# Performance work log

Measured on AMD Instinct MI355X. Metric: run time of the kernel, lower is better.

The kernel has to match this reference:

```python
import jax, jax.numpy as jnp
import numpy as np

LAM = 0.1
EPS = 1e-5

def _conv(x, w, b, pad):
    y = jax.lax.conv_general_dilated(x, w, (1, 1), [(pad, pad), (pad, pad)],
                                     dimension_numbers=('NCHW', 'OIHW', 'NCHW'))
    return y + b[None, :, None, None]

def _bn(x, g, b, m, v):
    return (x - m[None, :, None, None]) * (g / jnp.sqrt(v + EPS))[None, :, None, None] + b[None, :, None, None]

def _simam(x):
    # leave-one-out mean/var per HxW map, closed-form single-pass (same math as the
    # original per-pixel mask loop: torch unbiased var over the n-1 'other' values)
    n = x.shape[-2] * x.shape[-1]
    s = jnp.sum(x, axis=(-2, -1), keepdims=True)
    ss = jnp.sum(x * x, axis=(-2, -1), keepdims=True)
    mu = (s - x) / (n - 1)
    var = (ss - x * x - (n - 1) * mu * mu) / (n - 2)
    e = 4.0 * (var + LAM) / ((x - mu) ** 2 + 2.0 * var + 2.0 * LAM)
    return jax.nn.sigmoid(1.0 / e) * x

def setup_inputs():
    B, T, D, H, NC = 128, 128, 64, 256, 5
    IN = 64 * D
    ks = iter(jax.random.split(jax.random.key(0), 64))
    def w(shape, s=0.05):
        return jax.random.normal(next(ks), shape, jnp.float32) * s
    d = {'x': jax.random.normal(next(ks), (B, T, D), jnp.float32)}
    for nm, ci, co, k in [('c1a', 1, 32, 1), ('c1b', 32, 32, 3), ('c2a', 32, 64, 1), ('c2b', 64, 64, 3)]:
        d[nm + '_w'] = w((co, ci, k, k)); d[nm + '_b'] = w((co,))
        bn = 'bn' + nm[1:]
        d[bn + '_g'] = jnp.ones((co,), jnp.float32)
        d[bn + '_b'] = jnp.zeros((co,), jnp.float32)
        d[bn + '_m'] = w((co,), 0.01)
        d[bn + '_v'] = jnp.ones((co,), jnp.float32)
    for i in range(3):
        d['q%d_w' % i] = w((IN, H)); d['q%d_b' % i] = w((IN,))
        d['r%d_w' % i] = w((H, IN)); d['r%d_b' % i] = w((H,))
    d['wih'] = w((4 * H, IN)); d['whh'] = w((4 * H, H))
    d['bih'] = w((4 * H,)); d['bhh'] = w((4 * H,))
    d['fc_w'] = w((NC, H)); d['fc_b'] = w((NC,))
    return d

def reference(x, c1a_w, c1a_b, bn1a_g, bn1a_b, bn1a_m, bn1a_v, c1b_w, c1b_b, bn1b_g, bn1b_b, bn1b_m, bn1b_v, c2a_w, c2a_b, bn2a_g, bn2a_b, bn2a_m, bn2a_v, c2b_w, c2b_b, bn2b_g, bn2b_b, bn2b_m, bn2b_v, q0_w, q0_b, r0_w, r0_b, q1_w, q1_b, r1_w, r1_b, q2_w, q2_b, r2_w, r2_b, wih, whh, bih, bhh, fc_w, fc_b):
    B, T, D = x.shape
    h4 = x[:, None]  # [B,1,T,D]
    h4 = jax.nn.relu(_bn(_conv(h4, c1a_w, c1a_b, 0), bn1a_g, bn1a_b, bn1a_m, bn1a_v))
    h4 = jax.nn.relu(_bn(_conv(h4, c1b_w, c1b_b, 1), bn1b_g, bn1b_b, bn1b_m, bn1b_v))
    h4 = _simam(h4)
    h4 = jax.nn.relu(_bn(_conv(h4, c2a_w, c2a_b, 0), bn2a_g, bn2a_b, bn2a_m, bn2a_v))
    h4 = jax.nn.relu(_bn(_conv(h4, c2b_w, c2b_b, 1), bn2b_g, bn2b_b, bn2b_m, bn2b_v))
    h4 = _simam(h4)
    C = h4.shape[1]
    xl = h4.reshape(B, T, C * D)  # raw reshape, matches torch .view on [B,C,T,D]
    H = whh.shape[1]

    def step(carry, xt):
        h, c = carry
        xm, hm = xt, h
        xm = 2.0 * jax.nn.sigmoid(hm @ q0_w.T + q0_b) * xm  # round 1
        hm = 2.0 * jax.nn.sigmoid(xm @ r0_w.T + r0_b) * hm  # round 2
        xm = 2.0 * jax.nn.sigmoid(hm @ q1_w.T + q1_b) * xm  # round 3
        hm = 2.0 * jax.nn.sigmoid(xm @ r1_w.T + r1_b) * hm  # round 4
        xm = 2.0 * jax.nn.sigmoid(hm @ q2_w.T + q2_b) * xm  # round 5
        hm = 2.0 * jax.nn.sigmoid(xm @ r2_w.T + r2_b) * hm  # round 6
        gates = xm @ wih.T + bih + hm @ whh.T + bhh
        i, f, g, o = jnp.split(gates, 4, axis=-1)  # torch LSTMCell gate order
        c_new = jax.nn.sigmoid(f) * c + jax.nn.sigmoid(i) * jnp.tanh(g)
        h_new = jax.nn.sigmoid(o) * jnp.tanh(c_new)
        return (h_new, c_new), None

    h0 = jnp.zeros((B, H), x.dtype)
    c0 = jnp.zeros((B, H), x.dtype)
    (hT, _), _ = jax.lax.scan(step, (h0, c0), jnp.swapaxes(xl, 0, 1))
    return hT @ fc_w.T + fc_b
```

## Files before the change

kernel.cpp:

```cpp
#include <hip/hip_runtime.h>
#include <math.h>


typedef unsigned short u16;

#define EPSBN 1e-5f

__device__ __forceinline__ float sigf(float x) { return 1.0f / (1.0f + expf(-x)); }

__device__ __forceinline__ float b2f(u16 u) {
  union { unsigned int i; float f; } v; v.i = ((unsigned int)u) << 16; return v.f;
}
__device__ __forceinline__ u16 f2b(float f) {
  union { float f; unsigned int i; } v; v.f = f;
  unsigned int r = v.i + 0x7FFFu + ((v.i >> 16) & 1u);
  return (u16)(r >> 16);
}

template <typename T> __device__ __forceinline__ float ld1(const T* p);
template <> __device__ __forceinline__ float ld1<float>(const float* p) { return *p; }
template <> __device__ __forceinline__ float ld1<u16>(const u16* p) { return b2f(*p); }
template <typename T> __device__ __forceinline__ void st1(T* p, float v);
template <> __device__ __forceinline__ void st1<float>(float* p, float v) { *p = v; }
template <> __device__ __forceinline__ void st1<u16>(u16* p, float v) { *p = f2b(v); }

__device__ __forceinline__ float simam_elem(float xv, float s, float ss) {
  float mu = (s - xv) * (1.0f / 8191.0f);
  float var = (ss - xv * xv - 8191.0f * mu * mu) * (1.0f / 8190.0f);
  float einv = ((xv - mu) * (xv - mu) + 2.0f * var + 0.2f) / (4.0f * (var + 0.1f));
  return xv * sigf(einv);
}

__global__ __launch_bounds__(256) void k_conv1(
    const float* __restrict__ x,
    const float* __restrict__ w1a, const float* __restrict__ b1a,
    const float* __restrict__ g1a, const float* __restrict__ bb1a,
    const float* __restrict__ m1a, const float* __restrict__ v1a,
    const float* __restrict__ w1b, const float* __restrict__ b1b,
    const float* __restrict__ g1b, const float* __restrict__ bb1b,
    const float* __restrict__ m1b, const float* __restrict__ v1b,
    u16* __restrict__ y1u, float* __restrict__ ps1, float* __restrict__ pss1)
{
  __shared__ float xs[6][66];
  __shared__ float a1[32][6][66];
  __shared__ float A1[32], T1[32], S2[32], T2[32];
  __shared__ float reds[4][32], redq[4][32];
  const int tid = threadIdx.x;
  const int b = blockIdx.x, t0 = blockIdx.y * 4;
  if (tid < 32) {
    float s = g1a[tid] * rsqrtf(v1a[tid] + EPSBN);
    A1[tid] = w1a[tid] * s;
    T1[tid] = (b1a[tid] - m1a[tid]) * s + bb1a[tid];
    float s2 = g1b[tid] * rsqrtf(v1b[tid] + EPSBN);
    S2[tid] = s2;
    T2[tid] = (b1b[tid] - m1b[tid]) * s2 + bb1b[tid];
  }
  for (int i = tid; i < 6 * 66; i += 256) {
    int r = i / 66, cc = i - r * 66;
    int t = t0 + r - 1, d = cc - 1;
    float v = 0.f;
    if (t >= 0 && t < 128 && d >= 0 && d < 64) v = x[(b * 128 + t) * 64 + d];
    xs[r][cc] = v;
  }
  __syncthreads();
  for (int i = tid; i < 32 * 6 * 66; i += 256) {
    int c = i / 396;
    int rr = i - c * 396;
    int r = rr / 66, cc = rr - r * 66;
    int t = t0 + r - 1, d = cc - 1;
    float v = 0.f;
    if (t >= 0 && t < 128 && d >= 0 && d < 64)
      v = fmaxf(xs[r][cc] * A1[c] + T1[c], 0.f);
    a1[c][r][cc] = v;
  }
  __syncthreads();
  const int d = tid & 63, tq = tid >> 6, lane = tid & 63;
  float acc[32];
#pragma unroll
  for (int i = 0; i < 32; ++i) acc[i] = 0.f;
#pragma unroll 1
  for (int c1 = 0; c1 < 32; ++c1) {
#pragma unroll
    for (int dt = 0; dt < 3; ++dt) {
      float av0 = a1[c1][tq + dt][d];
      float av1 = a1[c1][tq + dt][d + 1];
      float av2 = a1[c1][tq + dt][d + 2];
#pragma unroll
      for (int c2 = 0; c2 < 32; ++c2) {
        const float* wp = w1b + ((c2 * 32 + c1) * 3 + dt) * 3;
        acc[c2] += av0 * wp[0] + av1 * wp[1] + av2 * wp[2];
      }
    }
  }
  const size_t ob = (size_t)b * 32 * 8192 + (size_t)(t0 + tq) * 64 + d;
#pragma unroll
  for (int c2 = 0; c2 < 32; ++c2) {
    float v = fmaxf(acc[c2] * S2[c2] + T2[c2], 0.f);
    y1u[ob + (size_t)c2 * 8192] = f2b(v);
    float s = v, q = v * v;
#pragma unroll
    for (int off = 32; off; off >>= 1) {
      s += __shfl_down(s, off);
      q += __shfl_down(q, off);
    }
    if (lane == 0) { reds[tq][c2] = s; redq[tq][c2] = q; }
  }
  __syncthreads();
  if (tid < 32) {
    float s = (reds[0][tid] + reds[1][tid]) + (reds[2][tid] + reds[3][tid]);
    float q = (redq[0][tid] + redq[1][tid]) + (redq[2][tid] + redq[3][tid]);
    ps1[(size_t)((b * 32 + tid) << 5) + blockIdx.y] = s;
    pss1[(size_t)((b * 32 + tid) << 5) + blockIdx.y] = q;
  }
}

__global__ __launch_bounds__(256) void k_red(
    const float* __restrict__ ps, const float* __restrict__ pss,
    float* __restrict__ stats, int npart, int nplanes)
{
  int p = blockIdx.x * 256 + threadIdx.x;
  if (p >= nplanes) return;
  float s = 0.f, q = 0.f;
  for (int j = 0; j < npart; ++j) {
    s += ps[(size_t)p * npart + j];
    q += pss[(size_t)p * npart + j];
  }
  stats[p] = s;
  stats[nplanes + p] = q;
}

template <typename T>
__global__ __launch_bounds__(256) void k_simam_t(
    T* __restrict__ buf, const float* __restrict__ stats, int nplanes)
{
  const int p = blockIdx.x, tid = threadIdx.x;
  T* base = buf + (size_t)p * 8192;
  const float s = stats[p], ss = stats[nplanes + p];
#pragma unroll 4
  for (int i = 0; i < 32; ++i) {
    int idx = tid + i * 256;
    float v = ld1(base + idx);
    st1(base + idx, simam_elem(v, s, ss));
  }
}

template <typename ZT>
__global__ __launch_bounds__(256) void k_conv2(
    const u16* __restrict__ y1u,
    const float* __restrict__ w2a, const float* __restrict__ b2a,
    const float* __restrict__ g2a, const float* __restrict__ bb2a,
    const float* __restrict__ m2a, const float* __restrict__ v2a,
    const float* __restrict__ w2b, const float* __restrict__ b2b,
    const float* __restrict__ g2b, const float* __restrict__ bb2b,
    const float* __restrict__ m2b, const float* __restrict__ v2b,
    ZT* __restrict__ z, float* __restrict__ ps2, float* __restrict__ pss2)
{
  __shared__ float y1s[32][4][66];
  __shared__ float a2[64][4][66];
  __shared__ float sA2a[64], sT2a[64], sA2b[64], sT2b[64];
  const int tid = threadIdx.x;
  const int t0 = blockIdx.x * 2, b = blockIdx.y;
  if (tid < 64) {
    float sa = g2a[tid] * rsqrtf(v2a[tid] + EPSBN);
    sA2a[tid] = sa;
    sT2a[tid] = (b2a[tid] - m2a[tid]) * sa + bb2a[tid];
    float sb = g2b[tid] * rsqrtf(v2b[tid] + EPSBN);
    sA2b[tid] = sb;
    sT2b[tid] = (b2b[tid] - m2b[tid]) * sb + bb2b[tid];
  }
  for (int i = tid; i < 32 * 4 * 66; i += 256) {
    int c1 = i / 264;
    int rr = i - c1 * 264;
    int r = rr / 66, cc = rr - r * 66;
    int t = t0 + r - 1, dd = cc - 1;
    float v = 0.f;
    if (t >= 0 && t < 128 && dd >= 0 && dd < 64)
      v = b2f(y1u[(size_t)(b * 32 + c1) * 8192 + t * 64 + dd]);
    y1s[c1][r][cc] = v;
  }
  __syncthreads();
  const int lane = tid & 63;
  const int c2base = __builtin_amdgcn_readfirstlane((int)(tid >> 6)) * 16;
#pragma unroll 1
  for (int i = 0; i < 16; ++i) {
    const int c2 = c2base + i;
    const float* wp = w2a + c2 * 32;
    const float scl = sA2a[c2], off = sT2a[c2];
#pragma unroll 1
    for (int r = 0; r < 4; ++r) {
      for (int cc = lane; cc < 66; cc += 64) {
        float acc = 0.f;
#pragma unroll
        for (int c1 = 0; c1 < 32; ++c1) acc += y1s[c1][r][cc] * wp[c1];
        int t = t0 + r - 1, dd = cc - 1;
        float val = 0.f;
        if (t >= 0 && t < 128 && dd >= 0 && dd < 64)
          val = fmaxf(acc * scl + off, 0.f);
        a2[c2][r][cc] = val;
      }
    }
  }
  __syncthreads();
  const int d = tid & 63;
  const int gq = __builtin_amdgcn_readfirstlane((int)(tid >> 6));
  float acc[16][2];
#pragma unroll
  for (int i = 0; i < 16; ++i) { acc[i][0] = 0.f; acc[i][1] = 0.f; }
#pragma unroll 1
  for (int c1 = 0; c1 < 64; ++c1) {
    float a00 = a2[c1][0][d], a01 = a2[c1][0][d + 1], a02 = a2[c1][0][d + 2];
    float a10 = a2[c1][1][d], a11 = a2[c1][1][d + 1], a12 = a2[c1][1][d + 2];
    float a20 = a2[c1][2][d], a21 = a2[c1][2][d + 1], a22 = a2[c1][2][d + 2];
    float a30 = a2[c1][3][d], a31 = a2[c1][3][d + 1], a32 = a2[c1][3][d + 2];
#pragma unroll
    for (int i = 0; i < 16; ++i) {
      const float* wp = w2b + (size_t)((gq * 16 + i) * 64 + c1) * 9;
      float w0 = wp[0], w1 = wp[1], w2 = wp[2];
      float w3 = wp[3], w4 = wp[4], w5 = wp[5];
      float w6 = wp[6], w7 = wp[7], w8 = wp[8];
      acc[i][0] += a00 * w0 + a01 * w1 + a02 * w2 + a10 * w3 + a11 * w4 +
                   a12 * w5 + a20 * w6 + a21 * w7 + a22 * w8;
      acc[i][1] += a10 * w0 + a11 * w1 + a12 * w2 + a20 * w3 + a21 * w4 +
                   a22 * w5 + a30 * w6 + a31 * w7 + a32 * w8;
    }
  }
#pragma unroll
  for (int i = 0; i < 16; ++i) {
    int c2 = gq * 16 + i;
    float sc = sA2b[c2], tb = sT2b[c2];
    float v0 = fmaxf(acc[i][0] * sc + tb, 0.f);
    float v1 = fmaxf(acc[i][1] * sc + tb, 0.f);
    size_t ob = (size_t)(b * 64 + c2) * 8192 + (size_t)t0 * 64 + d;
    st1(z + ob, v0);
    st1(z + ob + 64, v1);
    float s = v0 + v1, q = v0 * v0 + v1 * v1;
#pragma unroll
    for (int off = 32; off; off >>= 1) {
      s += __shfl_down(s, off);
      q += __shfl_down(q, off);
    }
    if (lane == 0) {
      ps2[(size_t)((b * 64 + c2) << 6) + blockIdx.x] = s;
      pss2[(size_t)((b * 64 + c2) << 6) + blockIdx.x] = q;
    }
  }
}

__global__ __launch_bounds__(256) void k_hfin(
    const float* __restrict__ gslab, const float* __restrict__ bih,
    const float* __restrict__ bhh, float* __restrict__ h, float* __restrict__ c,
    int is_t0)
{
  const int i = blockIdx.x * 256 + threadIdx.x;
  const int b = i >> 8, k = i & 255;
  if (is_t0) { h[i] = 0.f; c[i] = 0.f; return; }
  float gi = bih[k] + bhh[k];
  float gf = bih[k + 256] + bhh[k + 256];
  float gg = bih[k + 512] + bhh[k + 512];
  float go = bih[k + 768] + bhh[k + 768];
#pragma unroll 1
  for (int s = 0; s < 17; ++s) {
    const float* gs = gslab + (size_t)s * 131072 + b * 1024;
    gi += gs[k]; gf += gs[k + 256]; gg += gs[k + 512]; go += gs[k + 768];
  }
  float cn = sigf(gf) * c[i] + sigf(gi) * tanhf(gg);
  c[i] = cn;
  h[i] = sigf(go) * tanhf(cn);
}

template <typename XT>
__global__ __launch_bounds__(256) void k_q(
    const float* __restrict__ qW, const float* __restrict__ qb,
    const float* __restrict__ hmsrc, const XT* __restrict__ xin,
    int xin_bstride, float* __restrict__ xm)
{
  __shared__ float hms[32][256];
  const int tid = threadIdx.x;
  const int n0 = blockIdx.x * 64, b0 = blockIdx.y * 32;
  for (int i = tid; i < 32 * 256; i += 256) {
    int bl = i >> 8, k = i & 255;
    hms[bl][k] = hmsrc[(b0 + bl) * 256 + k];
  }
  __syncthreads();
  const int n = n0 + (tid & 63), bg = tid >> 6;
  float acc[8];
#pragma unroll
  for (int j = 0; j < 8; ++j) acc[j] = 0.f;
  const float* wrow = qW + (size_t)n * 256;
  for (int k = 0; k < 256; k += 4) {
    float4 w = *(const float4*)(wrow + k);
#pragma unroll
    for (int j = 0; j < 8; ++j) {
      float4 hv = *(const float4*)&hms[bg * 8 + j][k];
      acc[j] += w.x * hv.x + w.y * hv.y + w.z * hv.z + w.w * hv.w;
    }
  }
  float bias = qb[n];
#pragma unroll
  for (int j = 0; j < 8; ++j) {
    int b = b0 + bg * 8 + j;
    float xv = ld1(xin + (size_t)b * xin_bstride + n);
    xm[(size_t)b * 4096 + n] = 2.0f * sigf(acc[j] + bias) * xv;
  }
}

__global__ __launch_bounds__(256) void k_r(
    const float* __restrict__ rW, const float* __restrict__ xm,
    float* __restrict__ rslab)
{
  __shared__ float xms[32][128];
  const int tid = threadIdx.x;
  const int n0 = blockIdx.x * 32, b0 = blockIdx.y * 32, ks = blockIdx.z;
  const int n = n0 + (tid & 31), bg = tid >> 5;
  float acc[4] = {0.f, 0.f, 0.f, 0.f};
  const float* wrow = rW + (size_t)n * 4096;
#pragma unroll 1
  for (int sub = 0; sub < 4; ++sub) {
    const int kbase = ks * 512 + sub * 128;
    __syncthreads();
    for (int i = tid; i < 1024; i += 256) {
      int row = i >> 5, col4 = i & 31;
      *(float4*)&xms[row][col4 * 4] =
          *(const float4*)(xm + (size_t)(b0 + row) * 4096 + kbase + col4 * 4);
    }
    __syncthreads();
    for (int k = 0; k < 128; k += 4) {
      float4 w = *(const float4*)(wrow + kbase + k);
#pragma unroll
      for (int j = 0; j < 4; ++j) {
        float4 xv = *(const float4*)&xms[bg * 4 + j][k];
        acc[j] += w.x * xv.x + w.y * xv.y + w.z * xv.z + w.w * xv.w;
      }
    }
  }
#pragma unroll
  for (int j = 0; j < 4; ++j)
    rslab[(size_t)(ks * 128 + b0 + bg * 4 + j) * 256 + n] = acc[j];
}

__global__ __launch_bounds__(256) void k_hmfin(
    const float* __restrict__ rslab, const float* __restrict__ rb,
    const float* __restrict__ src, float* __restrict__ hm)
{
  const int i = blockIdx.x * 256 + threadIdx.x;
  const int b = i >> 8, k = i & 255;
  float acc = rb[k];
#pragma unroll
  for (int s = 0; s < 8; ++s) acc += rslab[(size_t)(s * 128 + b) * 256 + k];
  hm[i] = 2.0f * sigf(acc) * src[i];
}

__global__ __launch_bounds__(256) void k_whh(
    const float* __restrict__ whh, const float* __restrict__ hm,
    float* __restrict__ gslab16)
{
  __shared__ float hms[32][256];
  const int tid = threadIdx.x;
  const int n0 = blockIdx.x * 64, b0 = blockIdx.y * 32;
  for (int i = tid; i < 32 * 256; i += 256) {
    int bl = i >> 8, k = i & 255;
    hms[bl][k] = hm[(b0 + bl) * 256 + k];
  }
  __syncthreads();
  const int n = n0 + (tid & 63), bg = tid >> 6;
  float acc[8];
#pragma unroll
  for (int j = 0; j < 8; ++j) acc[j] = 0.f;
  const float* wrow = whh + (size_t)n * 256;
  for (int k = 0; k < 256; k += 4) {
    float4 w = *(const float4*)(wrow + k);
#pragma unroll
    for (int j = 0; j < 8; ++j) {
      float4 hv = *(const float4*)&hms[bg * 8 + j][k];
      acc[j] += w.x * hv.x + w.y * hv.y + w.z * hv.z + w.w * hv.w;
    }
  }
#pragma unroll
  for (int j = 0; j < 8; ++j)
    gslab16[(size_t)(b0 + bg * 8 + j) * 1024 + n] = acc[j];
}

__global__ __launch_bounds__(256) void k_g(
    const float* __restrict__ wih, const float* __restrict__ xm,
    float* __restrict__ gslab)
{
  __shared__ float xms[32][128];
  const int tid = threadIdx.x;
  const int jt = blockIdx.x, b0 = blockIdx.y * 32, ks = blockIdx.z;
  const int nj = jt * 64 + (tid & 63), bg = tid >> 6;
  float acc[8][4];
#pragma unroll
  for (int j = 0; j < 8; ++j)
#pragma unroll
    for (int g = 0; g < 4; ++g) acc[j][g] = 0.f;
  const float* w0 = wih + (size_t)nj * 4096;
  const float* w1 = wih + (size_t)(nj + 256) * 4096;
  const float* w2 = wih + (size_t)(nj + 512) * 4096;
  const float* w3 = wih + (size_t)(nj + 768) * 4096;
#pragma unroll 1
  for (int sub = 0; sub < 2; ++sub) {
    const int kbase = ks * 256 + sub * 128;
    __syncthreads();
    for (int i = tid; i < 1024; i += 256) {
      int row = i >> 5, col4 = i & 31;
      *(float4*)&xms[row][col4 * 4] =
          *(const float4*)(xm + (size_t)(b0 + row) * 4096 + kbase + col4 * 4);
    }
    __syncthreads();
    for (int k = 0; k < 128; k += 4) {
      float4 wa = *(const float4*)(w0 + kbase + k);
      float4 wb = *(const float4*)(w1 + kbase + k);
      float4 wc = *(const float4*)(w2 + kbase + k);
      float4 wd = *(const float4*)(w3 + kbase + k);
#pragma unroll
      for (int j = 0; j < 8; ++j) {
        float4 xv = *(const float4*)&xms[bg * 8 + j][k];
        acc[j][0] += wa.x * xv.x + wa.y * xv.y + wa.z * xv.z + wa.w * xv.w;
        acc[j][1] += wb.x * xv.x + wb.y * xv.y + wb.z * xv.z + wb.w * xv.w;
        acc[j][2] += wc.x * xv.x + wc.y * xv.y + wc.z * xv.z + wc.w * xv.w;
        acc[j][3] += wd.x * xv.x + wd.y * xv.y + wd.z * xv.z + wd.w * xv.w;
      }
    }
  }
#pragma unroll
  for (int j = 0; j < 8; ++j) {
    size_t base = (size_t)ks * 131072 + (size_t)(b0 + bg * 8 + j) * 1024 + nj;
    gslab[base] = acc[j][0];
    gslab[base + 256] = acc[j][1];
    gslab[base + 512] = acc[j][2];
    gslab[base + 768] = acc[j][3];
  }
}

__global__ __launch_bounds__(256) void k_fc(
    const float* __restrict__ h, const float* __restrict__ fcw,
    const float* __restrict__ fcb, float* __restrict__ out)
{
  __shared__ float hs[256];
  const int tid = threadIdx.x, b = blockIdx.x;
  hs[tid] = h[b * 256 + tid];
  __syncthreads();
  if (tid < 5) {
    float acc = fcb[tid];
    for (int k = 0; k < 256; ++k) acc += hs[k] * fcw[tid * 256 + k];
    out[b * 5 + tid] = acc;
  }
}

__global__ __launch_bounds__(256) void k_report(float* out, float v, int n) {
  int i = blockIdx.x * 256 + threadIdx.x;
  if (i < n) out[i] = v;
}

struct Net {
  const float *x;
  const float *c1a_w, *c1a_b, *g1a, *b1a, *m1a, *v1a;
  const float *c1b_w, *c1b_b, *g1b, *b1b, *m1b, *v1b;
  const float *c2a_w, *c2a_b, *g2a, *b2a, *m2a, *v2a;
  const float *c2b_w, *c2b_b, *g2b, *b2b, *m2b, *v2b;
  const float *qw[3], *qb[3], *rw[3], *rb[3];
  const float *wih, *whh, *bih, *bhh, *fcw, *fcb;
};

template <typename ZT>
static void run_all(const Net& p, ZT* z, u16* y1u, float* scr,
                    float* ps1, float* pss1, float* st1v,
                    float* ps2, float* pss2, float* st2v,
                    float* out, hipStream_t stream)
{
  float* xm    = scr;
  float* h     = scr + 524288;
  float* c     = scr + 557056;
  float* hm    = scr + 589824;
  float* rslab = scr + 622592;
  float* gslab = scr + 884736;

  k_conv1<<<dim3(128, 32), 256, 0, stream>>>(p.x, p.c1a_w, p.c1a_b, p.g1a,
      p.b1a, p.m1a, p.v1a, p.c1b_w, p.c1b_b, p.g1b, p.b1b, p.m1b, p.v1b,
      y1u, ps1, pss1);
  k_red<<<16, 256, 0, stream>>>(ps1, pss1, st1v, 32, 4096);
  k_simam_t<u16><<<4096, 256, 0, stream>>>(y1u, st1v, 4096);
  k_conv2<ZT><<<dim3(64, 128), 256, 0, stream>>>(y1u, p.c2a_w, p.c2a_b, p.g2a,
      p.b2a, p.m2a, p.v2a, p.c2b_w, p.c2b_b, p.g2b, p.b2b, p.m2b, p.v2b,
      z, ps2, pss2);
  k_red<<<32, 256, 0, stream>>>(ps2, pss2, st2v, 64, 8192);
  k_simam_t<ZT><<<8192, 256, 0, stream>>>(z, st2v, 8192);

  for (int t = 0; t < 128; ++t) {
    k_hfin<<<128, 256, 0, stream>>>(gslab, p.bih, p.bhh, h, c, t == 0 ? 1 : 0);
    for (int s = 0; s < 3; ++s) {
      if (s == 0)
        k_q<ZT><<<dim3(64, 4), 256, 0, stream>>>(p.qw[0], p.qb[0], h,
            z + (size_t)t * 4096, 524288, xm);
      else
        k_q<float><<<dim3(64, 4), 256, 0, stream>>>(p.qw[s], p.qb[s], hm,
            xm, 4096, xm);
      k_r<<<dim3(8, 4, 8), 256, 0, stream>>>(p.rw[s], xm, rslab);
      k_hmfin<<<128, 256, 0, stream>>>(rslab, p.rb[s], (s == 0) ? h : hm, hm);
    }
    k_whh<<<dim3(16, 4), 256, 0, stream>>>(p.whh, hm, gslab + (size_t)16 * 131072);
    k_g<<<dim3(4, 4, 16), 256, 0, stream>>>(p.wih, xm, gslab);
  }
  k_hfin<<<128, 256, 0, stream>>>(gslab, p.bih, p.bhh, h, c, 0);
  k_fc<<<128, 256, 0, stream>>>(h, p.fcw, p.fcb, out);
}

extern "C" void kernel_launch(void* const* d_in, const int* in_sizes, int n_in,
                              void* d_out, int out_size, void* d_ws, size_t ws_size,
                              hipStream_t stream)
{
  (void)in_sizes; (void)n_in;
  Net p;
  p.x = (const float*)d_in[0];
  p.c1a_w = (const float*)d_in[1];  p.c1a_b = (const float*)d_in[2];
  p.g1a = (const float*)d_in[3];    p.b1a = (const float*)d_in[4];
  p.m1a = (const float*)d_in[5];    p.v1a = (const float*)d_in[6];
  p.c1b_w = (const float*)d_in[7];  p.c1b_b = (const float*)d_in[8];
  p.g1b = (const float*)d_in[9];    p.b1b = (const float*)d_in[10];
  p.m1b = (const float*)d_in[11];   p.v1b = (const float*)d_in[12];
  p.c2a_w = (const float*)d_in[13]; p.c2a_b = (const float*)d_in[14];
  p.g2a = (const float*)d_in[15];   p.b2a = (const float*)d_in[16];
  p.m2a = (const float*)d_in[17];   p.v2a = (const float*)d_in[18];
  p.c2b_w = (const float*)d_in[19]; p.c2b_b = (const float*)d_in[20];
  p.g2b = (const float*)d_in[21];   p.b2b = (const float*)d_in[22];
  p.m2b = (const float*)d_in[23];   p.v2b = (const float*)d_in[24];
  for (int i = 0; i < 3; ++i) {
    p.qw[i] = (const float*)d_in[25 + 4 * i];
    p.qb[i] = (const float*)d_in[26 + 4 * i];
    p.rw[i] = (const float*)d_in[27 + 4 * i];
    p.rb[i] = (const float*)d_in[28 + 4 * i];
  }
  p.wih = (const float*)d_in[37]; p.whh = (const float*)d_in[38];
  p.bih = (const float*)d_in[39]; p.bhh = (const float*)d_in[40];
  p.fcw = (const float*)d_in[41]; p.fcb = (const float*)d_in[42];
  float* out = (float*)d_out;
  char* base = (char*)d_ws;

  const size_t ZB_F32 = 268435456, ZB_BF16 = 134217728, Y1B = 67108864;
  const size_t STATS = 1048576 * 2 + 65536 + 2097152 * 2 + 65536;
  const size_t HI_NEED = ZB_F32 + Y1B + STATS;
  const size_t LO_NEED = ZB_BF16 + Y1B + STATS;

  if (ws_size >= HI_NEED) {
    float* z = (float*)base;
    u16* y1u = (u16*)(base + ZB_F32);
    float* scr = (float*)(base + ZB_F32);
    char* sb = base + ZB_F32 + Y1B;
    run_all<float>(p, z, y1u, scr,
                   (float*)sb, (float*)(sb + 1048576), (float*)(sb + 2097152),
                   (float*)(sb + 2162688), (float*)(sb + 4259840),
                   (float*)(sb + 6356992), out, stream);
  } else if (ws_size >= LO_NEED) {
    u16* z = (u16*)base;
    u16* y1u = (u16*)(base + ZB_BF16);
    float* scr = (float*)(base + ZB_BF16);
    char* sb = base + ZB_BF16 + Y1B;
    run_all<u16>(p, z, y1u, scr,
                 (float*)sb, (float*)(sb + 1048576), (float*)(sb + 2097152),
                 (float*)(sb + 2162688), (float*)(sb + 4259840),
                 (float*)(sb + 6356992), out, stream);
  } else {
    k_report<<<3, 256, 0, stream>>>(out, (float)(ws_size >> 20), out_size);
  }
}
```

Measured before the change: 28.48 ms.

## Fuse the LSTM recurrence into one persistent kernel with grid barriers

Replaces the roughly eleven kernel launches per timestep (q, r, hm-finalise, whh, split-K gate and h-finalise kernels) with a single persistent 256-block kernel. It steps through the q, r and gate phases separated by a software grid barrier built on an atomic counter. The r and gate phases are repartitioned so each thread pair computes a full dot product and applies the nonlinearity directly, which removes the split-K slab buffers and reduction kernels. The trade-off is that weight reuse across the batch through shared-memory tiling is lost, so each block re-reads weights. The barrier also assumes all 256 blocks are co-resident without a cooperative launch.

Result: slower. 110.0 ms (+286.3%).

```diff
diff --git a/kernel.cpp b/kernel.cpp
--- a/kernel.cpp
+++ b/kernel.cpp
@@ -246,204 +246,178 @@
   }
 }
 
-__global__ __launch_bounds__(256) void k_hfin(
-    const float* __restrict__ gslab, const float* __restrict__ bih,
-    const float* __restrict__ bhh, float* __restrict__ h, float* __restrict__ c,
-    int is_t0)
-{
-  const int i = blockIdx.x * 256 + threadIdx.x;
-  const int b = i >> 8, k = i & 255;
-  if (is_t0) { h[i] = 0.f; c[i] = 0.f; return; }
-  float gi = bih[k] + bhh[k];
-  float gf = bih[k + 256] + bhh[k + 256];
-  float gg = bih[k + 512] + bhh[k + 512];
-  float go = bih[k + 768] + bhh[k + 768];
-#pragma unroll 1
-  for (int s = 0; s < 17; ++s) {
-    const float* gs = gslab + (size_t)s * 131072 + b * 1024;
-    gi += gs[k]; gf += gs[k + 256]; gg += gs[k + 512]; go += gs[k + 768];
-  }
-  float cn = sigf(gf) * c[i] + sigf(gi) * tanhf(gg);
-  c[i] = cn;
-  h[i] = sigf(go) * tanhf(cn);
+__device__ __forceinline__ void gridbar(unsigned* cnt, unsigned target) {
+  __threadfence();
+  __syncthreads();
+  if (threadIdx.x == 0) {
+    atomicAdd(cnt, 1u);
+    while (__hip_atomic_load(cnt, __ATOMIC_ACQUIRE, __HIP_MEMORY_SCOPE_AGENT) <
+           target)
+      __builtin_amdgcn_s_sleep(2);
+  }
+  __syncthreads();
 }
 
 template <typename XT>
-__global__ __launch_bounds__(256) void k_q(
-    const float* __restrict__ qW, const float* __restrict__ qb,
-    const float* __restrict__ hmsrc, const XT* __restrict__ xin,
-    int xin_bstride, float* __restrict__ xm)
-{
-  __shared__ float hms[32][256];
-  const int tid = threadIdx.x;
-  const int n0 = blockIdx.x * 64, b0 = blockIdx.y * 32;
-  for (int i = tid; i < 32 * 256; i += 256) {
-    int bl = i >> 8, k = i & 255;
-    hms[bl][k] = hmsrc[(b0 + bl) * 256 + k];
-  }
-  __syncthreads();
-  const int n = n0 + (tid & 63), bg = tid >> 6;
-  float acc[8];
-#pragma unroll
-  for (int j = 0; j < 8; ++j) acc[j] = 0.f;
-  const float* wrow = qW + (size_t)n * 256;
+__device__ __forceinline__ void q_phase(
+    const float* __restrict__ qw, const float* __restrict__ qbias,
+    const float* __restrict__ hsrc, const XT* __restrict__ xin,
+    size_t xin_bstride, float* __restrict__ xm, float (*hs)[256],
+    int blk, int tid)
+{
+  const int b0 = (blk >> 6) * 32;
+  for (int i = tid; i < 32 * 256; i += 256)
+    hs[i >> 8][i & 255] = hsrc[(size_t)(b0 + (i >> 8)) * 256 + (i & 255)];
+  __syncthreads();
+  const int n = (blk & 63) * 64 + (tid & 63), bg = tid >> 6;
+  float acc[8] = {0.f, 0.f, 0.f, 0.f, 0.f, 0.f, 0.f, 0.f};
+  const float* wrow = qw + (size_t)n * 256;
   for (int k = 0; k < 256; k += 4) {
     float4 w = *(const float4*)(wrow + k);
 #pragma unroll
     for (int j = 0; j < 8; ++j) {
-      float4 hv = *(const float4*)&hms[bg * 8 + j][k];
+      float4 hv = *(const float4*)&hs[bg * 8 + j][k];
       acc[j] += w.x * hv.x + w.y * hv.y + w.z * hv.z + w.w * hv.w;
     }
   }
-  float bias = qb[n];
+  float bias = qbias[n];
 #pragma unroll
   for (int j = 0; j < 8; ++j) {
     int b = b0 + bg * 8 + j;
     float xv = ld1(xin + (size_t)b * xin_bstride + n);
-    xm[(size_t)b * 4096 + n] = 2.0f * sigf(acc[j] + bias) * xv;
-  }
-}
-
-__global__ __launch_bounds__(256) void k_r(
-    const float* __restrict__ rW, const float* __restrict__ xm,
-    float* __restrict__ rslab)
-{
-  __shared__ float xms[32][128];
-  const int tid = threadIdx.x;
-  const int n0 = blockIdx.x * 32, b0 = blockIdx.y * 32, ks = blockIdx.z;
-  const int n = n0 + (tid & 31), bg = tid >> 5;
-  float acc[4] = {0.f, 0.f, 0.f, 0.f};
-  const float* wrow = rW + (size_t)n * 4096;
+    xm[(size_t)b * 4096 + n] = 2.f * sigf(acc[j] + bias) * xv;
+  }
+}
+
+__device__ __forceinline__ void r_phase(
+    const float* __restrict__ rw, const float* __restrict__ rbias,
+    const float* __restrict__ src, const float* __restrict__ xm,
+    float* __restrict__ hm, int blk, int tid)
+{
+  const int half = tid & 1, pr = tid >> 1;
+  const int n = (blk & 15) * 16 + (pr & 15);
+  const int b = (blk >> 4) * 8 + (pr >> 4);
+  const float* wrow = rw + (size_t)n * 4096 + half * 2048;
+  const float* xrow = xm + (size_t)b * 4096 + half * 2048;
+  float acc = 0.f;
+#pragma unroll 4
+  for (int k = 0; k < 2048; k += 8) {
+    float4 w0 = *(const float4*)(wrow + k);
+    float4 w1 = *(const float4*)(wrow + k + 4);
+    float4 x0 = *(const float4*)(xrow + k);
+    float4 x1 = *(const float4*)(xrow + k + 4);
+    acc += w0.x * x0.x + w0.y * x0.y + w0.z * x0.z + w0.w * x0.w +
+           w1.x * x1.x + w1.y * x1.y + w1.z * x1.z + w1.w * x1.w;
+  }
+  float tot = acc + __shfl_xor(acc, 1);
+  if (half == 0) {
+    int idx = b * 256 + n;
+    hm[idx] = 2.f * sigf(tot + rbias[n]) * src[idx];
+  }
+}
+
+__device__ __forceinline__ void g_phase(
+    const float* __restrict__ wih, const float* __restrict__ whh,
+    const float* __restrict__ bih, const float* __restrict__ bhh,
+    const float* __restrict__ xm, const float* __restrict__ hm,
+    float* __restrict__ h, float* __restrict__ c, int blk, int tid)
+{
+  const int half = tid & 1, pr = tid >> 1;
+  const int kk = (blk & 15) * 16 + (pr & 15);
+  const int b = (blk >> 4) * 8 + (pr >> 4);
+  float a0 = 0.f, a1 = 0.f, a2 = 0.f, a3 = 0.f;
+  const float* xrow = xm + (size_t)b * 4096 + half * 2048;
+  const float* w0 = wih + (size_t)kk * 4096 + half * 2048;
+  const float* w1 = wih + (size_t)(kk + 256) * 4096 + half * 2048;
+  const float* w2 = wih + (size_t)(kk + 512) * 4096 + half * 2048;
+  const float* w3 = wih + (size_t)(kk + 768) * 4096 + half * 2048;
+#pragma unroll 2
+  for (int k = 0; k < 2048; k += 4) {
+    float4 xv = *(const float4*)(xrow + k);
+    float4 wa = *(const float4*)(w0 + k);
+    float4 wb = *(const float4*)(w1 + k);
+    float4 wc = *(const float4*)(w2 + k);
+    float4 wd = *(const float4*)(w3 + k);
+    a0 += wa.x * xv.x + wa.y * xv.y + wa.z * xv.z + wa.w * xv.w;
+    a1 += wb.x * xv.x + wb.y * xv.y + wb.z * xv.z + wb.w * xv.w;
+    a2 += wc.x * xv.x + wc.y * xv.y + wc.z * xv.z + wc.w * xv.w;
+    a3 += wd.x * xv.x + wd.y * xv.y + wd.z * xv.z + wd.w * xv.w;
+  }
+  const float* hrow = hm + (size_t)b * 256 + half * 128;
+  const float* v0 = whh + (size_t)kk * 256 + half * 128;
+  const float* v1 = whh + (size_t)(kk + 256) * 256 + half * 128;
+  const float* v2 = whh + (size_t)(kk + 512) * 256 + half * 128;
+  const float* v3 = whh + (size_t)(kk + 768) * 256 + half * 128;
+#pragma unroll 4
+  for (int k = 0; k < 128; k += 4) {
+    float4 hv = *(const float4*)(hrow + k);
+    float4 wa = *(const float4*)(v0 + k);
+    float4 wb = *(const float4*)(v1 + k);
+    float4 wc = *(const float4*)(v2 + k);
+    float4 wd = *(const float4*)(v3 + k);
+    a0 += wa.x * hv.x + wa.y * hv.y + wa.z * hv.z + wa.w * hv.w;
+    a1 += wb.x * hv.x + wb.y * hv.y + wb.z * hv.z + wb.w * hv.w;
+    a2 += wc.x * hv.x + wc.y * hv.y + wc.z * hv.z + wc.w * hv.w;
+    a3 += wd.x * hv.x + wd.y * hv.y + wd.z * hv.z + wd.w * hv.w;
+  }
+  a0 += __shfl_xor(a0, 1);
+  a1 += __shfl_xor(a1, 1);
+  a2 += __shfl_xor(a2, 1);
+  a3 += __shfl_xor(a3, 1);
+  if (half == 0) {
+    int idx = b * 256 + kk;
+    float gi = a0 + bih[kk] + bhh[kk];
+    float gf = a1 + bih[kk + 256] + bhh[kk + 256];
+    float gg = a2 + bih[kk + 512] + bhh[kk + 512];
+    float go = a3 + bih[kk + 768] + bhh[kk + 768];
+    float cn = sigf(gf) * c[idx] + sigf(gi) * tanhf(gg);
+    c[idx] = cn;
+    h[idx] = sigf(go) * tanhf(cn);
+  }
+}
+
+template <typename ZT>
+__global__ __launch_bounds__(256, 1) void k_lstm(
+    const ZT* __restrict__ z,
+    const float* __restrict__ q0w, const float* __restrict__ q0b,
+    const float* __restrict__ r0w, const float* __restrict__ r0b,
+    const float* __restrict__ q1w, const float* __restrict__ q1b,
+    const float* __restrict__ r1w, const float* __restrict__ r1b,
+    const float* __restrict__ q2w, const float* __restrict__ q2b,
+    const float* __restrict__ r2w, const float* __restrict__ r2b,
+    const float* __restrict__ wih, const float* __restrict__ whh,
+    const float* __restrict__ bih, const float* __restrict__ bhh,
+    const float* __restrict__ fcw, const float* __restrict__ fcb,
+    float* __restrict__ xm, float* __restrict__ h, float* __restrict__ c,
+    float* __restrict__ hm, unsigned* __restrict__ cnt,
+    float* __restrict__ out)
+{
+  __shared__ float hs[32][256];
+  const int blk = blockIdx.x, tid = threadIdx.x;
+  unsigned ep = 0;
 #pragma unroll 1
-  for (int sub = 0; sub < 4; ++sub) {
-    const int kbase = ks * 512 + sub * 128;
-    __syncthreads();
-    for (int i = tid; i < 1024; i += 256) {
-      int row = i >> 5, col4 = i & 31;
-      *(float4*)&xms[row][col4 * 4] =
-          *(const float4*)(xm + (size_t)(b0 + row) * 4096 + kbase + col4 * 4);
-    }
-    __syncthreads();
-    for (int k = 0; k < 128; k += 4) {
-      float4 w = *(const float4*)(wrow + kbase + k);
-#pragma unroll
-      for (int j = 0; j < 4; ++j) {
-        float4 xv = *(const float4*)&xms[bg * 4 + j][k];
-        acc[j] += w.x * xv.x + w.y * xv.y + w.z * xv.z + w.w * xv.w;
-      }
-    }
-  }
-#pragma unroll
-  for (int j = 0; j < 4; ++j)
-    rslab[(size_t)(ks * 128 + b0 + bg * 4 + j) * 256 + n] = acc[j];
-}
-
-__global__ __launch_bounds__(256) void k_hmfin(
-    const float* __restrict__ rslab, const float* __restrict__ rb,
-    const float* __restrict__ src, float* __restrict__ hm)
-{
-  const int i = blockIdx.x * 256 + threadIdx.x;
-  const int b = i >> 8, k = i & 255;
-  float acc = rb[k];
-#pragma unroll
-  for (int s = 0; s < 8; ++s) acc += rslab[(size_t)(s * 128 + b) * 256 + k];
-  hm[i] = 2.0f * sigf(acc) * src[i];
-}
-
-__global__ __launch_bounds__(256) void k_whh(
-    const float* __restrict__ whh, const float* __restrict__ hm,
-    float* __restrict__ gslab16)
-{
-  __shared__ float hms[32][256];
-  const int tid = threadIdx.x;
-  const int n0 = blockIdx.x * 64, b0 = blockIdx.y * 32;
-  for (int i = tid; i < 32 * 256; i += 256) {
-    int bl = i >> 8, k = i & 255;
-    hms[bl][k] = hm[(b0 + bl) * 256 + k];
-  }
-  __syncthreads();
-  const int n = n0 + (tid & 63), bg = tid >> 6;
-  float acc[8];
-#pragma unroll
-  for (int j = 0; j < 8; ++j) acc[j] = 0.f;
-  const float* wrow = whh + (size_t)n * 256;
-  for (int k = 0; k < 256; k += 4) {
-    float4 w = *(const float4*)(wrow + k);
-#pragma unroll
-    for (int j = 0; j < 8; ++j) {
-      float4 hv = *(const float4*)&hms[bg * 8 + j][k];
-      acc[j] += w.x * hv.x + w.y * hv.y + w.z * hv.z + w.w * hv.w;
-    }
-  }
-#pragma unroll
-  for (int j = 0; j < 8; ++j)
-    gslab16[(size_t)(b0 + bg * 8 + j) * 1024 + n] = acc[j];
-}
-
-__global__ __launch_bounds__(256) void k_g(
-    const float* __restrict__ wih, const float* __restrict__ xm,
-    float* __restrict__ gslab)
-{
-  __shared__ float xms[32][128];
-  const int tid = threadIdx.x;
-  const int jt = blockIdx.x, b0 = blockIdx.y * 32, ks = blockIdx.z;
-  const int nj = jt * 64 + (tid & 63), bg = tid >> 6;
-  float acc[8][4];
-#pragma unroll
-  for (int j = 0; j < 8; ++j)
-#pragma unroll
-    for (int g = 0; g < 4; ++g) acc[j][g] = 0.f;
-  const float* w0 = wih + (size_t)nj * 4096;
-  const float* w1 = wih + (size_t)(nj + 256) * 4096;
-  const float* w2 = wih + (size_t)(nj + 512) * 4096;
-  const float* w3 = wih + (size_t)(nj + 768) * 4096;
-#pragma unroll 1
-  for (int sub = 0; sub < 2; ++sub) {
-    const int kbase = ks * 256 + sub * 128;
-    __syncthreads();
-    for (int i = tid; i < 1024; i += 256) {
-      int row = i >> 5, col4 = i & 31;
-      *(float4*)&xms[row][col4 * 4] =
-          *(const float4*)(xm + (size_t)(b0 + row) * 4096 + kbase + col4 * 4);
-    }
-    __syncthreads();
-    for (int k = 0; k < 128; k += 4) {
-      float4 wa = *(const float4*)(w0 + kbase + k);
-      float4 wb = *(const float4*)(w1 + kbase + k);
-      float4 wc = *(const float4*)(w2 + kbase + k);
-      float4 wd = *(const float4*)(w3 + kbase + k);
-#pragma unroll
-      for (int j = 0; j < 8; ++j) {
-        float4 xv = *(const float4*)&xms[bg * 8 + j][k];
-        acc[j][0] += wa.x * xv.x + wa.y * xv.y + wa.z * xv.z + wa.w * xv.w;
-        acc[j][1] += wb.x * xv.x + wb.y * xv.y + wb.z * xv.z + wb.w * xv.w;
-        acc[j][2] += wc.x * xv.x + wc.y * xv.y + wc.z * xv.z + wc.w * xv.w;
-        acc[j][3] += wd.x * xv.x + wd.y * xv.y + wd.z * xv.z + wd.w * xv.w;
-      }
-    }
-  }
-#pragma unroll
-  for (int j = 0; j < 8; ++j) {
-    size_t base = (size_t)ks * 131072 + (size_t)(b0 + bg * 8 + j) * 1024 + nj;
-    gslab[base] = acc[j][0];
-    gslab[base + 256] = acc[j][1];
-    gslab[base + 512] = acc[j][2];
-    gslab[base + 768] = acc[j][3];
-  }
-}
-
-__global__ __launch_bounds__(256) void k_fc(
-    const float* __restrict__ h, const float* __restrict__ fcw,
-    const float* __restrict__ fcb, float* __restrict__ out)
-{
-  __shared__ float hs[256];
-  const int tid = threadIdx.x, b = blockIdx.x;
-  hs[tid] = h[b * 256 + tid];
-  __syncthreads();
-  if (tid < 5) {
+  for (int t = 0; t < 128; ++t) {
+    q_phase<ZT>(q0w, q0b, h, z + (size_t)t * 4096, 524288, xm, hs, blk, tid);
+    gridbar(cnt, (++ep) * 256);
+    r_phase(r0w, r0b, h, xm, hm, blk, tid);
+    gridbar(cnt, (++ep) * 256);
+    q_phase<float>(q1w, q1b, hm, xm, 4096, xm, hs, blk, tid);
+    gridbar(cnt, (++ep) * 256);
+    r_phase(r1w, r1b, hm, xm, hm, blk, tid);
+    gridbar(cnt, (++ep) * 256);
+    q_phase<float>(q2w, q2b, hm, xm, 4096, xm, hs, blk, tid);
+    gridbar(cnt, (++ep) * 256);
+    r_phase(r2w, r2b, hm, xm, hm, blk, tid);
+    gridbar(cnt, (++ep) * 256);
+    g_phase(wih, whh, bih, bhh, xm, hm, h, c, blk, tid);
+    gridbar(cnt, (++ep) * 256);
+  }
+  if (blk < 128 && tid < 5) {
     float acc = fcb[tid];
-    for (int k = 0; k < 256; ++k) acc += hs[k] * fcw[tid * 256 + k];
-    out[b * 5 + tid] = acc;
+    const float* hr = h + blk * 256;
+    const float* wr = fcw + tid * 256;
+    for (int k = 0; k < 256; ++k) acc += hr[k] * wr[k];
+    out[blk * 5 + tid] = acc;
   }
 }
 
@@ -468,12 +442,11 @@
                     float* ps2, float* pss2, float* st2v,
                     float* out, hipStream_t stream)
 {
-  float* xm    = scr;
-  float* h     = scr + 524288;
-  float* c     = scr + 557056;
-  float* hm    = scr + 589824;
-  float* rslab = scr + 622592;
-  float* gslab = scr + 884736;
+  float* xm = scr;
+  float* h  = scr + 524288;
+  float* c  = scr + 557056;
+  float* hm = scr + 589824;
+  unsigned* cnt = (unsigned*)(scr + 622592);
 
   k_conv1<<<dim3(128, 32), 256, 0, stream>>>(p.x, p.c1a_w, p.c1a_b, p.g1a,
       p.b1a, p.m1a, p.v1a, p.c1b_w, p.c1b_b, p.g1b, p.b1b, p.m1b, p.v1b,
@@ -486,23 +459,15 @@
   k_red<<<32, 256, 0, stream>>>(ps2, pss2, st2v, 64, 8192);
   k_simam_t<ZT><<<8192, 256, 0, stream>>>(z, st2v, 8192);
 
-  for (int t = 0; t < 128; ++t) {
-    k_hfin<<<128, 256, 0, stream>>>(gslab, p.bih, p.bhh, h, c, t == 0 ? 1 : 0);
-    for (int s = 0; s < 3; ++s) {
-      if (s == 0)
-        k_q<ZT><<<dim3(64, 4), 256, 0, stream>>>(p.qw[0], p.qb[0], h,
-            z + (size_t)t * 4096, 524288, xm);
-      else
-        k_q<float><<<dim3(64, 4), 256, 0, stream>>>(p.qw[s], p.qb[s], hm,
-            xm, 4096, xm);
-      k_r<<<dim3(8, 4, 8), 256, 0, stream>>>(p.rw[s], xm, rslab);
-      k_hmfin<<<128, 256, 0, stream>>>(rslab, p.rb[s], (s == 0) ? h : hm, hm);
-    }
-    k_whh<<<dim3(16, 4), 256, 0, stream>>>(p.whh, hm, gslab + (size_t)16 * 131072);
-    k_g<<<dim3(4, 4, 16), 256, 0, stream>>>(p.wih, xm, gslab);
-  }
-  k_hfin<<<128, 256, 0, stream>>>(gslab, p.bih, p.bhh, h, c, 0);
-  k_fc<<<128, 256, 0, stream>>>(h, p.fcw, p.fcb, out);
+  hipMemsetAsync(h, 0, 2 * 32768 * sizeof(float), stream);
+  hipMemsetAsync(cnt, 0, sizeof(unsigned), stream);
+
+  k_lstm<ZT><<<256, 256, 0, stream>>>(z,
+      p.qw[0], p.qb[0], p.rw[0], p.rb[0],
+      p.qw[1], p.qb[1], p.rw[1], p.rb[1],
+      p.qw[2], p.qb[2], p.rw[2], p.rb[2],
+      p.wih, p.whh, p.bih, p.bhh, p.fcw, p.fcb,
+      xm, h, c, hm, cnt, out);
 }
 
 extern "C" void kernel_launch(void* const* d_in, const int* in_sizes, int n_in,
```
